# Performance work log

Hardware: AMD Instinct MI355X
Metric: run time of the kernel (lower is better)

Reference implementation:

```python
import jax, jax.numpy as jnp
import numpy as np

L = 2        # lstm layers (encoder == decoder, required since h0/c0 are shared)
H = 512      # neural_size
FEAT = 128   # encoder input feature size
T_ENC = 512  # encoder sequence length
B = 512      # batch
PRED_LEN = 96


def _lstm_cell(x, h, c, W_ih, W_hh, b_ih, b_hh):
    # PyTorch gate order: i, f, g, o
    gates = x @ W_ih.T + b_ih + h @ W_hh.T + b_hh
    i, f, g, o = jnp.split(gates, 4, axis=-1)
    i = jax.nn.sigmoid(i)
    f = jax.nn.sigmoid(f)
    g = jnp.tanh(g)
    o = jax.nn.sigmoid(o)
    c_new = f * c + i * g
    h_new = o * jnp.tanh(c_new)
    return h_new, c_new


def _multilayer_step(layer_params, x, h, c):
    # h, c: [L, B, H]; x: [B, in]; loop over fixed small layer count
    hs, cs = [], []
    inp = x
    for l, (W_ih, W_hh, b_ih, b_hh) in enumerate(layer_params):
        h_new, c_new = _lstm_cell(inp, h[l], c[l], W_ih, W_hh, b_ih, b_hh)
        hs.append(h_new)
        cs.append(c_new)
        inp = h_new
    return inp, jnp.stack(hs), jnp.stack(cs)


def setup_inputs() -> dict:
    key = jax.random.key(0)
    ks = jax.random.split(key, 24)
    s = 0.1  # weight init scale
    inp = {
        "X_encode": jax.random.normal(ks[0], (B, T_ENC, FEAT), jnp.float32),
        "X_decode": jax.random.normal(ks[1], (B, PRED_LEN, 8), jnp.float32),
        "y": jax.random.normal(ks[2], (B, PRED_LEN, 1), jnp.float32),
        "tf_mask": jax.random.randint(ks[3], (PRED_LEN,), 0, 2, jnp.int32),
    }
    # encoder LSTM params (layer 0 in=FEAT, layer 1 in=H)
    inp["enc_W_ih0"] = jax.random.normal(ks[4], (4 * H, FEAT), jnp.float32) * s
    inp["enc_W_hh0"] = jax.random.normal(ks[5], (4 * H, H), jnp.float32) * s
    inp["enc_b_ih0"] = jax.random.normal(ks[6], (4 * H,), jnp.float32) * s
    inp["enc_b_hh0"] = jax.random.normal(ks[7], (4 * H,), jnp.float32) * s
    inp["enc_W_ih1"] = jax.random.normal(ks[8], (4 * H, H), jnp.float32) * s
    inp["enc_W_hh1"] = jax.random.normal(ks[9], (4 * H, H), jnp.float32) * s
    inp["enc_b_ih1"] = jax.random.normal(ks[10], (4 * H,), jnp.float32) * s
    inp["enc_b_hh1"] = jax.random.normal(ks[11], (4 * H,), jnp.float32) * s
    # decoder LSTM params (layer 0 in=1, layer 1 in=H)
    inp["dec_W_ih0"] = jax.random.normal(ks[12], (4 * H, 1), jnp.float32) * s
    inp["dec_W_hh0"] = jax.random.normal(ks[13], (4 * H, H), jnp.float32) * s
    inp["dec_b_ih0"] = jax.random.normal(ks[14], (4 * H,), jnp.float32) * s
    inp["dec_b_hh0"] = jax.random.normal(ks[15], (4 * H,), jnp.float32) * s
    inp["dec_W_ih1"] = jax.random.normal(ks[16], (4 * H, H), jnp.float32) * s
    inp["dec_W_hh1"] = jax.random.normal(ks[17], (4 * H, H), jnp.float32) * s
    inp["dec_b_ih1"] = jax.random.normal(ks[18], (4 * H,), jnp.float32) * s
    inp["dec_b_hh1"] = jax.random.normal(ks[19], (4 * H,), jnp.float32) * s
    # output projection
    inp["fc_W"] = jax.random.normal(ks[20], (1, H), jnp.float32) * s
    inp["fc_b"] = jax.random.normal(ks[21], (1,), jnp.float32) * s
    return inp


def reference(X_encode, X_decode, y, tf_mask,
              enc_W_ih0, enc_W_hh0, enc_b_ih0, enc_b_hh0,
              enc_W_ih1, enc_W_hh1, enc_b_ih1, enc_b_hh1,
              dec_W_ih0, dec_W_hh0, dec_b_ih0, dec_b_hh0,
              dec_W_ih1, dec_W_hh1, dec_b_ih1, dec_b_hh1,
              fc_W, fc_b):
    enc_params = [(enc_W_ih0, enc_W_hh0, enc_b_ih0, enc_b_hh0),
                  (enc_W_ih1, enc_W_hh1, enc_b_ih1, enc_b_hh1)]
    dec_params = [(dec_W_ih0, dec_W_hh0, dec_b_ih0, dec_b_hh0),
                  (dec_W_ih1, dec_W_hh1, dec_b_ih1, dec_b_hh1)]

    batch = X_encode.shape[0]
    h0 = jnp.zeros((L, batch, H), X_encode.dtype)
    c0 = jnp.zeros((L, batch, H), X_encode.dtype)

    # ---- encoder: scan over time, keep only final (h, c) ----
    def enc_step(carry, x_t):
        h, c = carry
        _, h, c = _multilayer_step(enc_params, x_t, h, c)
        return (h, c), None

    (h, c), _ = jax.lax.scan(enc_step, (h0, c0), jnp.swapaxes(X_encode, 0, 1))

    # ---- decoder initial input: sum(sum(X_decode, 1), 1).unsqueeze(-1) ----
    dec_in0 = jnp.sum(X_decode, axis=(1, 2))[:, None]  # (B, 1)

    # teacher forcing: y[:, t+1, :] when tf and t < pred_len-1, else own output
    y_next = jnp.concatenate([y[:, 1:, :], jnp.zeros_like(y[:, :1, :])], axis=1)
    tf = (tf_mask != 0) & (jnp.arange(PRED_LEN) < PRED_LEN - 1)

    def dec_step(carry, xs):
        inp, h, c = carry
        tf_t, y_t = xs  # scalar bool, (B, 1)
        top, h, c = _multilayer_step(dec_params, inp, h, c)
        out = top @ fc_W.T + fc_b  # (B, 1)
        nxt = jnp.where(tf_t, y_t, out)
        return (nxt, h, c), out

    _, outs = jax.lax.scan(dec_step, (dec_in0, h, c),
                           (tf, jnp.swapaxes(y_next, 0, 1)))
    final_out = jnp.swapaxes(outs, 0, 1)  # (B, pred_len, 1)
    return final_out
```

## Files before the change

kernel.cpp:

```cpp
#include <hip/hip_runtime.h>


typedef unsigned int u32;
typedef unsigned short u16;

using bf16x8  = __attribute__((ext_vector_type(8))) __bf16;
using u16x8   = __attribute__((ext_vector_type(8))) u16;
using floatx4 = __attribute__((ext_vector_type(4))) float;

#define NWG 256
#define HB  262144

#define ENC0_REG (128 * 2 * 640)
#define ENC1_REG (128 * 2 * 1024)
#define DEC0_REG (128 * 2 * 512)
#define DEC1_REG (128 * 2 * 1024)

#define H0_CHUNK 0
#define H1_CHUNK 4096
#define LO_BYTES 32768

#define AS1C(p) ((const __attribute__((address_space(1))) void*)(p))
#define AS3(p)  ((__attribute__((address_space(3))) void*)(u32)(size_t)(p))

__device__ __forceinline__ u16 f2bf(float f) {
  u32 u = __builtin_bit_cast(u32, f);
  u += 0x7FFFu + ((u >> 16) & 1u);
  return (u16)(u >> 16);
}
__device__ __forceinline__ float bf2f(u16 h) {
  return __builtin_bit_cast(float, (u32)h << 16);
}
__device__ __forceinline__ bf16x8 ld8(const u16* p) {
  return __builtin_bit_cast(bf16x8, *reinterpret_cast<const u16x8*>(p));
}
__device__ __forceinline__ float sig_(float x) {
  x = fminf(fmaxf(x, -30.f), 30.f);
  return 1.f / (1.f + __expf(-x));
}
__device__ __forceinline__ float tanh_(float x) {
  x = fminf(fmaxf(x, -15.f), 15.f);
  float e = __expf(2.f * x);
  return (e - 1.f) / (e + 1.f);
}

#define MFMA(a, b, c) __builtin_amdgcn_mfma_f32_16x16x32_bf16((a), (b), (c), 0, 0, 0)

__device__ __forceinline__ void gemm_lds(floatx4* acc, const char* apb,
    const u16* __restrict__ Wreg, int strideW,
    int lj0, int l15, int quad, int kbeg, int kend)
{
  const u16* wp = Wreg + (size_t)(lj0 + l15) * 2 * strideW + (quad << 3);
  const size_t gs = (size_t)strideW << 6;
  #pragma unroll 2
  for (int k = kbeg; k < kend; k += 32) {
    const int kb8 = ((k >> 3) + quad) << 9;
    bf16x8 ah = *reinterpret_cast<const bf16x8*>(apb + kb8);
    bf16x8 al = *reinterpret_cast<const bf16x8*>(apb + kb8 + LO_BYTES);
    #pragma unroll
    for (int g = 0; g < 4; ++g) {
      bf16x8 wh = ld8(wp + k + g * gs);
      bf16x8 wl = ld8(wp + k + g * gs + strideW);
      acc[g] = MFMA(ah, wh, acc[g]);
      acc[g] = MFMA(ah, wl, acc[g]);
      acc[g] = MFMA(al, wh, acc[g]);
    }
  }
}

__device__ __forceinline__ void gemm_x128s(floatx4* acc,
    const float* __restrict__ X, int t,
    const u16* __restrict__ Wreg, int strideW,
    int row0, int lj0, int lane)
{
  const int quad = lane >> 4, l15 = lane & 15;
  const float* xp = X + ((size_t)(row0 + l15) * 512 + t) * 128 + (quad << 3);
  const u16* wp = Wreg + (size_t)(lj0 + l15) * 2 * strideW + (quad << 3);
  const size_t gs = (size_t)strideW << 6;
  #pragma unroll
  for (int k = 0; k < 128; k += 32) {
    floatx4 xa = *reinterpret_cast<const floatx4*>(xp + k);
    floatx4 xb_ = *reinterpret_cast<const floatx4*>(xp + k + 4);
    u16x8 uh, ul;
    #pragma unroll
    for (int i = 0; i < 4; ++i) {
      u16 h0 = f2bf(xa[i]);  uh[i] = h0;     ul[i] = f2bf(xa[i] - bf2f(h0));
      u16 h1 = f2bf(xb_[i]); uh[4 + i] = h1; ul[4 + i] = f2bf(xb_[i] - bf2f(h1));
    }
    bf16x8 ah = __builtin_bit_cast(bf16x8, uh);
    bf16x8 al = __builtin_bit_cast(bf16x8, ul);
    #pragma unroll
    for (int g = 0; g < 4; ++g) {
      bf16x8 wh = ld8(wp + k + g * gs);
      bf16x8 wl = ld8(wp + k + g * gs + strideW);
      acc[g] = MFMA(ah, wh, acc[g]);
      acc[g] = MFMA(ah, wl, acc[g]);
      acc[g] = MFMA(al, wh, acc[g]);
    }
  }
}

__device__ __forceinline__ void store_h_split(u16* __restrict__ hout,
                                              size_t off, float h) {
  u16 hh = f2bf(h);
  u16 hl = f2bf(h - bf2f(hh));
  __hip_atomic_store(hout + off,      hh, __ATOMIC_RELAXED, __HIP_MEMORY_SCOPE_AGENT);
  __hip_atomic_store(hout + off + HB, hl, __ATOMIC_RELAXED, __HIP_MEMORY_SCOPE_AGENT);
}

__device__ __forceinline__ void cell_store(const floatx4* acc,
    float* __restrict__ c, u16* __restrict__ hout,
    const float* __restrict__ bs, int row0, int j0, int lane)
{
  const int quad = lane >> 4, l15 = lane & 15;
  const int col = j0 + l15;
  const float bi = bs[col], bff = bs[512 + col], bg = bs[1024 + col], bo = bs[1536 + col];
  const int r0 = row0 + (quad << 2);
  #pragma unroll
  for (int r = 0; r < 4; ++r) {
    const size_t off = ((size_t)(r0 + r) << 9) + col;
    float ii = sig_(acc[0][r] + bi);
    float ff = sig_(acc[1][r] + bff);
    float gg = tanh_(acc[2][r] + bg);
    float oo = sig_(acc[3][r] + bo);
    float cn = ff * c[off] + ii * gg;
    c[off] = cn;
    store_h_split(hout, off, oo * tanh_(cn));
  }
}

__device__ __forceinline__ void cell_store_dec0(const floatx4* acc,
    float* __restrict__ c, u16* __restrict__ hout,
    const float* __restrict__ bs, const float* __restrict__ w0col,
    const float* __restrict__ din0, const float* __restrict__ y,
    const int* __restrict__ tfm, float* __restrict__ dout,
    int t, int row0, int j0, int lane)
{
  const int quad = lane >> 4, l15 = lane & 15;
  const int col = j0 + l15;
  const float bi = bs[col], bff = bs[512 + col], bg = bs[1024 + col], bo = bs[1536 + col];
  const float wi = w0col[col], wf = w0col[512 + col], wg = w0col[1024 + col], wo = w0col[1536 + col];
  const int r0 = row0 + (quad << 2);
  #pragma unroll
  for (int r = 0; r < 4; ++r) {
    const int row = r0 + r;
    float inp;
    if (t == 0) inp = din0[row];
    else if (tfm[t - 1] != 0) inp = y[row * 96 + t];
    else inp = __hip_atomic_load(dout + row * 96 + (t - 1),
                                 __ATOMIC_RELAXED, __HIP_MEMORY_SCOPE_AGENT);
    const size_t off = ((size_t)row << 9) + col;
    float ii = sig_(acc[0][r] + bi + inp * wi);
    float ff = sig_(acc[1][r] + bff + inp * wf);
    float gg = tanh_(acc[2][r] + bg + inp * wg);
    float oo = sig_(acc[3][r] + bo + inp * wo);
    float cn = ff * c[off] + ii * gg;
    c[off] = cn;
    store_h_split(hout, off, oo * tanh_(cn));
  }
}

__device__ __forceinline__ void cell_store_dec1(const floatx4* acc,
    float* __restrict__ c, u16* __restrict__ hout,
    const float* __restrict__ bs, const float* __restrict__ fcW,
    const float* __restrict__ fcb, float* __restrict__ dout,
    int t, int row0, int j0, int lane)
{
  const int quad = lane >> 4, l15 = lane & 15;
  const int col = j0 + l15;
  const float bi = bs[col], bff = bs[512 + col], bg = bs[1024 + col], bo = bs[1536 + col];
  const float fw = fcW[col];
  const int r0 = row0 + (quad << 2);
  float s[4];
  #pragma unroll
  for (int r = 0; r < 4; ++r) {
    const size_t off = ((size_t)(r0 + r) << 9) + col;
    float ii = sig_(acc[0][r] + bi);
    float ff = sig_(acc[1][r] + bff);
    float gg = tanh_(acc[2][r] + bg);
    float oo = sig_(acc[3][r] + bo);
    float cn = ff * c[off] + ii * gg;
    c[off] = cn;
    float h = oo * tanh_(cn);
    store_h_split(hout, off, h);
    s[r] = h * fw;
  }
  #pragma unroll
  for (int m = 1; m < 16; m <<= 1) {
    #pragma unroll
    for (int r = 0; r < 4; ++r) s[r] += __shfl_xor(s[r], m, 64);
  }
  if (l15 == 0) {
    #pragma unroll
    for (int r = 0; r < 4; ++r) {
      float v = s[r];
      if (j0 == 0) v += fcb[0];
      atomicAdd(&dout[(size_t)(r0 + r) * 96 + t], v);
    }
  }
}

__global__ __launch_bounds__(512) void seq2seq_persist(
    const float* __restrict__ Xenc, const float* __restrict__ y,
    const int* __restrict__ tfm, const float* __restrict__ dWih0col,
    const float* __restrict__ fcW, const float* __restrict__ fcb,
    const u16* __restrict__ enc0, const u16* __restrict__ enc1,
    const u16* __restrict__ dec0w, const u16* __restrict__ dec1,
    u16* __restrict__ h0bufs, u16* __restrict__ h1bufs,
    float* __restrict__ c0, float* __restrict__ c1,
    const float* __restrict__ bsum, const float* __restrict__ din0,
    float* __restrict__ dout, u32* __restrict__ bar)
{
  extern __shared__ char smem_c[];
  const int tid = threadIdx.x;
  const int g = blockIdx.x;
  const int wave = tid >> 6, lane = tid & 63;
  const int w4 = wave & 3, kh = wave >> 2;
  const int quad = lane >> 4, l15 = lane & 15;
  const int q = g >> 3;
  const int hj_tile = (g & 7) + ((q & 1) << 3);
  const int b_tile = q >> 1;
  const int b0 = b_tile << 5, hj0 = hj_tile << 5;
  const int row0 = b0 + ((w4 & 1) << 4);
  const int j0 = hj0 + ((w4 >> 1) << 4);
  const int lj0 = (w4 >> 1) << 4;
  u16* h0buf[2] = { h0bufs, h0bufs + 2 * HB };
  u16* h1buf[2] = { h1bufs, h1bufs + 2 * HB };
  unsigned ep = 0;

  const u16* enc0r = enc0  + (size_t)hj_tile * ENC0_REG;
  const u16* enc1r = enc1  + (size_t)hj_tile * ENC1_REG;
  const u16* dec0r = dec0w + (size_t)hj_tile * DEC0_REG;
  const u16* dec1r = dec1  + (size_t)hj_tile * DEC1_REG;

  const int lrow = ((w4 & 1) << 4) + l15;
  const char* apb0 = smem_c + lrow * 16;
  const char* apb1 = smem_c + 65536 + lrow * 16;
  floatx4* xb = (floatx4*)smem_c;
  #define XR(w4_, L_, g_) (((((w4_) * 2 + (L_)) * 4 + (g_)) << 6) + lane)

  auto stage = [&](const u16* hbuf, int region_chunk) {
    #pragma unroll
    for (int blk = 0; blk < 8; ++blk) {
      const int cw = (blk << 9) + (wave << 6);
      const int c  = cw + lane;
      const int half = c >> 11, cc = c & 2047;
      const int k8 = cc >> 5, row = cc & 31;
      const u16* src = hbuf + (size_t)half * HB
                     + ((size_t)(b0 + row) << 9) + (k8 << 3);
      __builtin_amdgcn_global_load_lds(
          AS1C(src), AS3(smem_c + (size_t)(region_chunk + cw) * 16),
          16, 0, 0x11 );
    }
  };

  auto gbar = [&]() {
    __syncthreads();
    ++ep;
    if (tid == 0) {
      __hip_atomic_fetch_add(&bar[b_tile * 64], 1u,
                             __ATOMIC_RELAXED, __HIP_MEMORY_SCOPE_AGENT);
      while (__hip_atomic_load(&bar[b_tile * 64],
                 __ATOMIC_RELAXED, __HIP_MEMORY_SCOPE_AGENT) < ep * 16u)
        __builtin_amdgcn_s_sleep(1);
    }
    asm volatile("" ::: "memory");
    __syncthreads();
  };

  for (int p = 0; p <= 512; ++p) {
    const int cur = p & 1, nxt = cur ^ 1;
    stage(h0buf[cur], H0_CHUNK);
    stage(h1buf[cur], H1_CHUNK);
    __syncthreads();
    floatx4 a1[4] = { floatx4{0,0,0,0}, floatx4{0,0,0,0}, floatx4{0,0,0,0}, floatx4{0,0,0,0} };
    floatx4 a0[4] = { floatx4{0,0,0,0}, floatx4{0,0,0,0}, floatx4{0,0,0,0}, floatx4{0,0,0,0} };
    if (p >= 1) {
      if (kh == 0) {
        gemm_lds(a1, apb0, enc1r,       1024, lj0, l15, quad, 0, 256);
        gemm_lds(a1, apb1, enc1r + 512, 1024, lj0, l15, quad, 0, 256);
      } else {
        gemm_lds(a1, apb0, enc1r,       1024, lj0, l15, quad, 256, 512);
        gemm_lds(a1, apb1, enc1r + 512, 1024, lj0, l15, quad, 256, 512);
      }
    }
    if (p <= 511) {
      if (kh == 0) {
        gemm_x128s(a0, Xenc, p, enc0r, 640, row0, lj0, lane);
        gemm_lds(a0, apb0, enc0r + 128, 640, lj0, l15, quad, 0, 192);
      } else {
        gemm_lds(a0, apb0, enc0r + 128, 640, lj0, l15, quad, 192, 512);
      }
    }
    __syncthreads();
    if (kh == 1) {
      for (int gg = 0; gg < 4; ++gg) xb[XR(w4, 0, gg)] = a1[gg];
      for (int gg = 0; gg < 4; ++gg) xb[XR(w4, 1, gg)] = a0[gg];
    }
    __syncthreads();
    if (kh == 0) {
      if (p >= 1) {
        for (int gg = 0; gg < 4; ++gg) a1[gg] += xb[XR(w4, 0, gg)];
        cell_store(a1, c1, h1buf[nxt], bsum + 2048, row0, j0, lane);
      }
      if (p <= 511) {
        for (int gg = 0; gg < 4; ++gg) a0[gg] += xb[XR(w4, 1, gg)];
        cell_store(a0, c0, h0buf[nxt], bsum, row0, j0, lane);
      }
    }
    gbar();
  }

  int cur0 = 0, cur1 = 1;
  for (int t = 0; t < 96; ++t) {
    {
      stage(h0buf[cur0], H0_CHUNK);
      __syncthreads();
      floatx4 acc[4] = { floatx4{0,0,0,0}, floatx4{0,0,0,0}, floatx4{0,0,0,0}, floatx4{0,0,0,0} };
      if (kh == 0) gemm_lds(acc, apb0, dec0r, 512, lj0, l15, quad, 0, 256);
      else         gemm_lds(acc, apb0, dec0r, 512, lj0, l15, quad, 256, 512);
      __syncthreads();
      if (kh == 1) {
        for (int gg = 0; gg < 4; ++gg) xb[XR(w4, 0, gg)] = acc[gg];
      }
      __syncthreads();
      if (kh == 0) {
        for (int gg = 0; gg < 4; ++gg) acc[gg] += xb[XR(w4, 0, gg)];
        cell_store_dec0(acc, c0, h0buf[cur0 ^ 1], bsum + 4096, dWih0col,
                        din0, y, tfm, dout, t, row0, j0, lane);
      }
    }
    gbar();
    cur0 ^= 1;
    {
      stage(h0buf[cur0], H0_CHUNK);
      stage(h1buf[cur1], H1_CHUNK);
      __syncthreads();
      floatx4 acc[4] = { floatx4{0,0,0,0}, floatx4{0,0,0,0}, floatx4{0,0,0,0}, floatx4{0,0,0,0} };
      if (kh == 0) {
        gemm_lds(acc, apb0, dec1r,       1024, lj0, l15, quad, 0, 256);
        gemm_lds(acc, apb1, dec1r + 512, 1024, lj0, l15, quad, 0, 256);
      } else {
        gemm_lds(acc, apb0, dec1r,       1024, lj0, l15, quad, 256, 512);
        gemm_lds(acc, apb1, dec1r + 512, 1024, lj0, l15, quad, 256, 512);
      }
      __syncthreads();
      if (kh == 1) {
        for (int gg = 0; gg < 4; ++gg) xb[XR(w4, 0, gg)] = acc[gg];
      }
      __syncthreads();
      if (kh == 0) {
        for (int gg = 0; gg < 4; ++gg) acc[gg] += xb[XR(w4, 0, gg)];
        cell_store_dec1(acc, c1, h1buf[cur1 ^ 1], bsum + 6144, fcW, fcb,
                        dout, t, row0, j0, lane);
      }
    }
    gbar();
    cur1 ^= 1;
  }
}

__global__ void prep_misc(float* c0, float* c1, u16* h0b, u16* h1b,
    float* dout, u32* bar, float* bsum,
    const float* ebih0, const float* ebhh0, const float* ebih1, const float* ebhh1,
    const float* dbih0, const float* dbhh0, const float* dbih1, const float* dbhh1,
    const float* Xdec, float* din0)
{
  const int idx = blockIdx.x * 256 + threadIdx.x;
  c0[idx] = 0.f; c1[idx] = 0.f;
  h0b[idx] = 0; h0b[idx + HB] = 0; h0b[idx + 2 * HB] = 0; h0b[idx + 3 * HB] = 0;
  h1b[idx] = 0; h1b[idx + HB] = 0; h1b[idx + 2 * HB] = 0; h1b[idx + 3 * HB] = 0;
  if (idx < 49152) dout[idx] = 0.f;
  if (idx < 8192) {
    const int which = idx >> 11, j = idx & 2047;
    float v;
    if (which == 0)      v = ebih0[j] + ebhh0[j];
    else if (which == 1) v = ebih1[j] + ebhh1[j];
    else if (which == 2) v = dbih0[j] + dbhh0[j];
    else                 v = dbih1[j] + dbhh1[j];
    bsum[idx] = v;
  }
  if (idx < 512) {
    float s = 0.f;
    const float* p = Xdec + (size_t)idx * 768;
    for (int i = 0; i < 768; ++i) s += p[i];
    din0[idx] = s;
  }
  if (idx < 1024) bar[idx] = 0u;
}

__device__ __forceinline__ void wsplit2(u16* dst, int S, int j_src, int k, float w) {
  const int j = j_src & 511, gg = j_src >> 9;
  const int hj = j >> 5, lj = j & 31;
  const size_t base = (size_t)((hj << 7) + (gg << 5) + lj) * 2 * S + k;
  u16 hh = f2bf(w);
  dst[base] = hh;
  dst[base + S] = f2bf(w - bf2f(hh));
}

__global__ void prep_weights(u16* enc0, const float* eWih0, const float* eWhh0,
    u16* enc1, const float* eWih1, const float* eWhh1,
    u16* dec0, const float* dWhh0,
    u16* dec1, const float* dWih1, const float* dWhh1)
{
  const int idx = blockIdx.x * 256 + threadIdx.x;
  if (idx < 2048 * 640) {
    const int j = idx / 640, k = idx - j * 640;
    wsplit2(enc0, 640, j, k,
            k < 128 ? eWih0[j * 128 + k] : eWhh0[j * 512 + (k - 128)]);
  }
  {
    const int j = idx >> 10, k = idx & 1023;
    wsplit2(enc1, 1024, j, k,
            k < 512 ? eWih1[(j << 9) + k] : eWhh1[(j << 9) + k - 512]);
    wsplit2(dec1, 1024, j, k,
            k < 512 ? dWih1[(j << 9) + k] : dWhh1[(j << 9) + k - 512]);
  }
  if (idx < 2048 * 512) {
    const int j = idx >> 9, k = idx & 511;
    wsplit2(dec0, 512, j, k, dWhh0[idx]);
  }
}

extern "C" void kernel_launch(void* const* d_in, const int* in_sizes, int n_in,
                              void* d_out, int out_size, void* d_ws, size_t ws_size,
                              hipStream_t stream)
{
  const float* Xenc  = (const float*)d_in[0];
  const float* Xdec  = (const float*)d_in[1];
  const float* y     = (const float*)d_in[2];
  const int*   tfm   = (const int*)d_in[3];
  const float* eWih0 = (const float*)d_in[4];
  const float* eWhh0 = (const float*)d_in[5];
  const float* ebih0 = (const float*)d_in[6];
  const float* ebhh0 = (const float*)d_in[7];
  const float* eWih1 = (const float*)d_in[8];
  const float* eWhh1 = (const float*)d_in[9];
  const float* ebih1 = (const float*)d_in[10];
  const float* ebhh1 = (const float*)d_in[11];
  const float* dWih0 = (const float*)d_in[12];
  const float* dWhh0 = (const float*)d_in[13];
  const float* dbih0 = (const float*)d_in[14];
  const float* dbhh0 = (const float*)d_in[15];
  const float* dWih1 = (const float*)d_in[16];
  const float* dWhh1 = (const float*)d_in[17];
  const float* dbih1 = (const float*)d_in[18];
  const float* dbhh1 = (const float*)d_in[19];
  const float* fcW   = (const float*)d_in[20];
  const float* fcb   = (const float*)d_in[21];
  float* dout = (float*)d_out;

  char* base = (char*)d_ws;
  size_t off = 0;
  auto alloc = [&](size_t n) -> char* {
    char* p = base + off;
    off = (off + n + 255) & ~(size_t)255;
    return p;
  };
  u32* bar  = (u32*)alloc(1024 * 4);
  u16* enc0 = (u16*)alloc((size_t)ENC0_REG * 16 * 2);
  u16* enc1 = (u16*)alloc((size_t)ENC1_REG * 16 * 2);
  u16* dec0 = (u16*)alloc((size_t)DEC0_REG * 16 * 2);
  u16* dec1 = (u16*)alloc((size_t)DEC1_REG * 16 * 2);
  u16* h0b  = (u16*)alloc((size_t)4 * HB * 2);
  u16* h1b  = (u16*)alloc((size_t)4 * HB * 2);
  float* c0 = (float*)alloc((size_t)HB * 4);
  float* c1 = (float*)alloc((size_t)HB * 4);
  float* bs = (float*)alloc((size_t)8192 * 4);
  float* di = (float*)alloc((size_t)512 * 4);

  static int lds_attr_set = 0;
  if (!lds_attr_set) {
    (void)hipFuncSetAttribute((const void*)seq2seq_persist,
        hipFuncAttributeMaxDynamicSharedMemorySize, 131072);
    lds_attr_set = 1;
  }

  prep_misc<<<1024, 256, 0, stream>>>(c0, c1, h0b, h1b, dout, bar, bs,
      ebih0, ebhh0, ebih1, ebhh1, dbih0, dbhh0, dbih1, dbhh1, Xdec, di);
  prep_weights<<<8192, 256, 0, stream>>>(enc0, eWih0, eWhh0, enc1, eWih1, eWhh1,
      dec0, dWhh0, dec1, dWih1, dWhh1);
  seq2seq_persist<<<NWG, 512, 131072, stream>>>(Xenc, y, tfm, dWih0, fcW, fcb,
      enc0, enc1, dec0, dec1, h0b, h1b, c0, c1, bs, di, dout, bar);
}
```

Baseline: 34.37 ms.

## Split K reduction across four wave groups using 1024-thread blocks

Each workgroup grows from 512 to 1024 threads, and the GEMM K dimension is split four ways instead of two. The three extra wave groups write partial sums to LDS and group 0 reduces them before the cell update. Staging loops shrink to match the larger thread count. The aim is to cut per-step latency in the serial recurrence by putting more waves on each step's GEMM. The cost is more LDS reduction traffic, extra __syncthreads, and higher register pressure under launch_bounds(1024).

Measured after the change: 39.62 ms. 15.3% more time.

```diff
diff --git a/kernel.cpp b/kernel.cpp
--- a/kernel.cpp
+++ b/kernel.cpp
@@ -200,7 +200,7 @@
   }
 }
 
-__global__ __launch_bounds__(512) void seq2seq_persist(
+__global__ __launch_bounds__(1024) void seq2seq_persist(
     const float* __restrict__ Xenc, const float* __restrict__ y,
     const int* __restrict__ tfm, const float* __restrict__ dWih0col,
     const float* __restrict__ fcW, const float* __restrict__ fcb,
@@ -215,7 +215,7 @@
   const int tid = threadIdx.x;
   const int g = blockIdx.x;
   const int wave = tid >> 6, lane = tid & 63;
-  const int w4 = wave & 3, kh = wave >> 2;
+  const int w4 = wave & 3, kq = wave >> 2;
   const int quad = lane >> 4, l15 = lane & 15;
   const int q = g >> 3;
   const int hj_tile = (g & 7) + ((q & 1) << 3);
@@ -237,12 +237,12 @@
   const char* apb0 = smem_c + lrow * 16;
   const char* apb1 = smem_c + 65536 + lrow * 16;
   floatx4* xb = (floatx4*)smem_c;
-  #define XR(w4_, L_, g_) (((((w4_) * 2 + (L_)) * 4 + (g_)) << 6) + lane)
+  #define XR(r_, w4_, g_) (((((r_) * 4 + (w4_)) * 4 + (g_)) << 6) + lane)
 
   auto stage = [&](const u16* hbuf, int region_chunk) {
     #pragma unroll
-    for (int blk = 0; blk < 8; ++blk) {
-      const int cw = (blk << 9) + (wave << 6);
+    for (int blk = 0; blk < 4; ++blk) {
+      const int cw = (blk << 10) + (wave << 6);
       const int c  = cw + lane;
       const int half = c >> 11, cc = c & 2047;
       const int k8 = cc >> 5, row = cc & 31;
@@ -276,37 +276,38 @@
     floatx4 a1[4] = { floatx4{0,0,0,0}, floatx4{0,0,0,0}, floatx4{0,0,0,0}, floatx4{0,0,0,0} };
     floatx4 a0[4] = { floatx4{0,0,0,0}, floatx4{0,0,0,0}, floatx4{0,0,0,0}, floatx4{0,0,0,0} };
     if (p >= 1) {
-      if (kh == 0) {
-        gemm_lds(a1, apb0, enc1r,       1024, lj0, l15, quad, 0, 256);
-        gemm_lds(a1, apb1, enc1r + 512, 1024, lj0, l15, quad, 0, 256);
+      const int kb = kq << 7;
+      gemm_lds(a1, apb0, enc1r,       1024, lj0, l15, quad, kb, kb + 128);
+      gemm_lds(a1, apb1, enc1r + 512, 1024, lj0, l15, quad, kb, kb + 128);
+    }
+    if (p <= 511) {
+      if (kq == 0) {
+        gemm_x128s(a0, Xenc, p, enc0r, 640, row0, lj0, lane);
+        gemm_lds(a0, apb0, enc0r + 128, 640, lj0, l15, quad, 0, 32);
       } else {
-        gemm_lds(a1, apb0, enc1r,       1024, lj0, l15, quad, 256, 512);
-        gemm_lds(a1, apb1, enc1r + 512, 1024, lj0, l15, quad, 256, 512);
+        const int kb = 32 + ((kq - 1) * 160);
+        gemm_lds(a0, apb0, enc0r + 128, 640, lj0, l15, quad, kb, kb + 160);
       }
     }
-    if (p <= 511) {
-      if (kh == 0) {
-        gemm_x128s(a0, Xenc, p, enc0r, 640, row0, lj0, lane);
-        gemm_lds(a0, apb0, enc0r + 128, 640, lj0, l15, quad, 0, 192);
-      } else {
-        gemm_lds(a0, apb0, enc0r + 128, 640, lj0, l15, quad, 192, 512);
-      }
-    }
-    __syncthreads();
-    if (kh == 1) {
-      for (int gg = 0; gg < 4; ++gg) xb[XR(w4, 0, gg)] = a1[gg];
-      for (int gg = 0; gg < 4; ++gg) xb[XR(w4, 1, gg)] = a0[gg];
-    }
-    __syncthreads();
-    if (kh == 0) {
-      if (p >= 1) {
-        for (int gg = 0; gg < 4; ++gg) a1[gg] += xb[XR(w4, 0, gg)];
-        cell_store(a1, c1, h1buf[nxt], bsum + 2048, row0, j0, lane);
-      }
-      if (p <= 511) {
-        for (int gg = 0; gg < 4; ++gg) a0[gg] += xb[XR(w4, 1, gg)];
-        cell_store(a0, c0, h0buf[nxt], bsum, row0, j0, lane);
-      }
+    __syncthreads();
+    if (kq) {
+      for (int gg = 0; gg < 4; ++gg) xb[XR(kq - 1, w4, gg)] = a1[gg];
+    }
+    __syncthreads();
+    if (!kq && p >= 1) {
+      for (int r = 0; r < 3; ++r)
+        for (int gg = 0; gg < 4; ++gg) a1[gg] += xb[XR(r, w4, gg)];
+      cell_store(a1, c1, h1buf[nxt], bsum + 2048, row0, j0, lane);
+    }
+    __syncthreads();
+    if (kq) {
+      for (int gg = 0; gg < 4; ++gg) xb[XR(kq - 1, w4, gg)] = a0[gg];
+    }
+    __syncthreads();
+    if (!kq && p <= 511) {
+      for (int r = 0; r < 3; ++r)
+        for (int gg = 0; gg < 4; ++gg) a0[gg] += xb[XR(r, w4, gg)];
+      cell_store(a0, c0, h0buf[nxt], bsum, row0, j0, lane);
     }
     gbar();
   }
@@ -317,15 +318,16 @@
       stage(h0buf[cur0], H0_CHUNK);
       __syncthreads();
       floatx4 acc[4] = { floatx4{0,0,0,0}, floatx4{0,0,0,0}, floatx4{0,0,0,0}, floatx4{0,0,0,0} };
-      if (kh == 0) gemm_lds(acc, apb0, dec0r, 512, lj0, l15, quad, 0, 256);
-      else         gemm_lds(acc, apb0, dec0r, 512, lj0, l15, quad, 256, 512);
-      __syncthreads();
-      if (kh == 1) {
-        for (int gg = 0; gg < 4; ++gg) xb[XR(w4, 0, gg)] = acc[gg];
+      const int kb = kq << 7;
+      gemm_lds(acc, apb0, dec0r, 512, lj0, l15, quad, kb, kb + 128);
+      __syncthreads();
+      if (kq) {
+        for (int gg = 0; gg < 4; ++gg) xb[XR(kq - 1, w4, gg)] = acc[gg];
       }
       __syncthreads();
-      if (kh == 0) {
-        for (int gg = 0; gg < 4; ++gg) acc[gg] += xb[XR(w4, 0, gg)];
+      if (!kq) {
+        for (int r = 0; r < 3; ++r)
+          for (int gg = 0; gg < 4; ++gg) acc[gg] += xb[XR(r, w4, gg)];
         cell_store_dec0(acc, c0, h0buf[cur0 ^ 1], bsum + 4096, dWih0col,
                         din0, y, tfm, dout, t, row0, j0, lane);
       }
@@ -337,20 +339,17 @@
       stage(h1buf[cur1], H1_CHUNK);
       __syncthreads();
       floatx4 acc[4] = { floatx4{0,0,0,0}, floatx4{0,0,0,0}, floatx4{0,0,0,0}, floatx4{0,0,0,0} };
-      if (kh == 0) {
-        gemm_lds(acc, apb0, dec1r,       1024, lj0, l15, quad, 0, 256);
-        gemm_lds(acc, apb1, dec1r + 512, 1024, lj0, l15, quad, 0, 256);
-      } else {
-        gemm_lds(acc, apb0, dec1r,       1024, lj0, l15, quad, 256, 512);
-        gemm_lds(acc, apb1, dec1r + 512, 1024, lj0, l15, quad, 256, 512);
+      const int kb = kq << 7;
+      gemm_lds(acc, apb0, dec1r,       1024, lj0, l15, quad, kb, kb + 128);
+      gemm_lds(acc, apb1, dec1r + 512, 1024, lj0, l15, quad, kb, kb + 128);
+      __syncthreads();
+      if (kq) {
+        for (int gg = 0; gg < 4; ++gg) xb[XR(kq - 1, w4, gg)] = acc[gg];
       }
       __syncthreads();
-      if (kh == 1) {
-        for (int gg = 0; gg < 4; ++gg) xb[XR(w4, 0, gg)] = acc[gg];
-      }
-      __syncthreads();
-      if (kh == 0) {
-        for (int gg = 0; gg < 4; ++gg) acc[gg] += xb[XR(w4, 0, gg)];
+      if (!kq) {
+        for (int r = 0; r < 3; ++r)
+          for (int gg = 0; gg < 4; ++gg) acc[gg] += xb[XR(r, w4, gg)];
         cell_store_dec1(acc, c1, h1buf[cur1 ^ 1], bsum + 6144, fcW, fcb,
                         dout, t, row0, j0, lane);
       }
@@ -480,6 +479,6 @@
       ebih0, ebhh0, ebih1, ebhh1, dbih0, dbhh0, dbih1, dbhh1, Xdec, di);
   prep_weights<<<8192, 256, 0, stream>>>(enc0, eWih0, eWhh0, enc1, eWih1, eWhh1,
       dec0, dWhh0, dec1, dWih1, dWhh1);
-  seq2seq_persist<<<NWG, 512, 131072, stream>>>(Xenc, y, tfm, dWih0, fcW, fcb,
+  seq2seq_persist<<<NWG, 1024, 131072, stream>>>(Xenc, y, tfm, dWih0, fcW, fcb,
       enc0, enc1, dec0, dec1, h0b, h1b, c0, c1, bs, di, dout, bar);
 }
```
